# Kernel tuning notes

Hardware: AMD Instinct MI355X
Metric: run time of the kernel (lower is better)

Reference implementation:

```python
import jax, jax.numpy as jnp
import numpy as np

T = 96      # CONTEXT_SIZE
B = 32      # BATCH_SIZE
DIN = 256   # input_dim
H = 512     # hidden_dim
V = 128     # output_dim (vocab)


def setup_inputs() -> dict:
    key = jax.random.key(0)
    ks = jax.random.split(key, 16)
    s_in = 1.0 / np.sqrt(DIN)
    s_h = 1.0 / np.sqrt(H)

    def u(k, shape, s):
        return jax.random.uniform(k, shape, jnp.float32, -s, s)

    return {
        "x": jax.random.normal(ks[0], (B, T, DIN), jnp.float32),
        # input->hidden gate weights (no bias), one per timestep: [T, H, DIN]
        "Wif": u(ks[1], (T, H, DIN), s_in),
        "Wii": u(ks[2], (T, H, DIN), s_in),
        "Wic": u(ks[3], (T, H, DIN), s_in),
        "Wio": u(ks[4], (T, H, DIN), s_in),
        # hidden->hidden gate weights (+bias), one per timestep: [T, H, H], [T, H]
        "Whf_w": u(ks[5], (T, H, H), s_h), "Whf_b": u(ks[6], (T, H), s_h),
        "Whi_w": u(ks[7], (T, H, H), s_h), "Whi_b": u(ks[8], (T, H), s_h),
        "Whc_w": u(ks[9], (T, H, H), s_h), "Whc_b": u(ks[10], (T, H), s_h),
        "Who_w": u(ks[11], (T, H, H), s_h), "Who_b": u(ks[12], (T, H), s_h),
        # per-step output projections: [T, V, H], [T, V]
        "lin_w": u(ks[13], (T, V, H), s_h), "lin_b": u(ks[14], (T, V), s_h),
    }


def reference(x, Wif, Wii, Wic, Wio, Whf_w, Whf_b, Whi_w, Whi_b,
              Whc_w, Whc_b, Who_w, Who_b, lin_w, lin_b):
    sig = jax.nn.sigmoid

    # --- step 0: h_prev/c_prev are None -> hidden-path linears (and their
    # biases) are entirely absent, and c_t = i * c_bar (no forget term).
    x0 = x[:, 0]                                    # [B, DIN]
    i0 = sig(x0 @ Wii[0].T)
    cb0 = jnp.tanh(x0 @ Wic[0].T)
    o0 = sig(x0 @ Wio[0].T)
    c0 = i0 * cb0
    h0 = o0 * jnp.tanh(c0)                          # [B, H]
    logit0 = h0 @ lin_w[0].T + lin_b[0]             # [B, V]

    # --- steps 1..T-1: full gated update, distinct weights per step.
    def step(carry, ws):
        c, h = carry
        (xt, wif, whfw, whfb, wii, whiw, whib,
         wic, whcw, whcb, wio, whow, whob, lw, lb) = ws
        f = sig(xt @ wif.T + h @ whfw.T + whfb)
        i = sig(xt @ wii.T + h @ whiw.T + whib)
        cb = jnp.tanh(xt @ wic.T + h @ whcw.T + whcb)
        o = sig(xt @ wio.T + h @ whow.T + whob)
        c_t = f * c + i * cb
        h_t = o * jnp.tanh(c_t)
        return (c_t, h_t), h_t @ lw.T + lb

    xs = (jnp.swapaxes(x, 0, 1)[1:],               # [T-1, B, DIN]
          Wif[1:], Whf_w[1:], Whf_b[1:],
          Wii[1:], Whi_w[1:], Whi_b[1:],
          Wic[1:], Whc_w[1:], Whc_b[1:],
          Wio[1:], Who_w[1:], Who_b[1:],
          lin_w[1:], lin_b[1:])
    _, logits_rest = jax.lax.scan(step, (c0, h0), xs)   # [T-1, B, V]

    logits = jnp.concatenate([logit0[None], logits_rest], axis=0)  # [T, B, V]
    # original stacks [B, 1, V] per step along dim=1 -> [B, T, 1, V]
    return jnp.transpose(logits, (1, 0, 2))[:, :, None, :]
```

## Files before the change

### kernel.cpp

```cpp
#include <hip/hip_runtime.h>
#include <hip/hip_bf16.h>

#define TT 96
#define BB 32
#define DIN 256
#define HH 512
#define VV 128
#define NB 256

#define BAR() asm volatile("s_waitcnt lgkmcnt(0)\ns_barrier" ::: "memory")

__global__ __launch_bounds__(256) void phaseA_kernel(
    const float* __restrict__ x,
    const float* __restrict__ Wf, const float* __restrict__ Wi,
    const float* __restrict__ Wc, const float* __restrict__ Wo,
    float* __restrict__ Z)
{
    int bid  = blockIdx.x;
    int t    = bid >> 4;
    int tile = bid & 15;
    int g    = tile >> 2;
    int h0   = (tile & 3) * 128;
    const float* W = (g == 0) ? Wf : (g == 1) ? Wi : (g == 2) ? Wc : Wo;

    __shared__ float4 Xs4[32 * 64];
    __shared__ float4 Wc4[128 * 8];

    int tid = threadIdx.x;
    {
        int b   = tid >> 3;
        int kq8 = tid & 7;
        const float* src = x + ((size_t)b * TT + t) * DIN;
        int bx = b & 15;
        #pragma unroll
        for (int j = 0; j < 8; ++j) {
            int q = kq8 * 8 + j;
            Xs4[b * 64 + (q ^ bx)] = *reinterpret_cast<const float4*>(src + q * 4);
        }
    }

    int rg = tid >> 3;
    int bg = tid & 7;
    const float* wbase = W + ((size_t)t * HH + h0) * DIN;

    int srow[4], sgq[4];
    #pragma unroll
    for (int j = 0; j < 4; ++j) {
        int s = j * 256 + tid;
        srow[j] = s >> 3;
        sgq[j]  = (s & 7) ^ ((srow[j] >> 2) & 7);
    }

    float4 stg[4];
    #pragma unroll
    for (int j = 0; j < 4; ++j)
        stg[j] = *reinterpret_cast<const float4*>(wbase + (size_t)srow[j] * DIN + sgq[j] * 4);

    float acc[4][4];
    #pragma unroll
    for (int r = 0; r < 4; ++r)
        #pragma unroll
        for (int c = 0; c < 4; ++c) acc[r][c] = 0.f;

    for (int kc = 0; kc < 8; ++kc) {
        __syncthreads();
        #pragma unroll
        for (int j = 0; j < 4; ++j) Wc4[j * 256 + tid] = stg[j];
        __syncthreads();
        if (kc < 7) {
            #pragma unroll
            for (int j = 0; j < 4; ++j)
                stg[j] = *reinterpret_cast<const float4*>(
                    wbase + (size_t)srow[j] * DIN + (kc + 1) * 32 + sgq[j] * 4);
        }
        #pragma unroll
        for (int q = 0; q < 8; ++q) {
            float4 xv[4], wv[4];
            #pragma unroll
            for (int c = 0; c < 4; ++c) {
                int b = c * 8 + bg;
                xv[c] = Xs4[b * 64 + ((kc * 8 + q) ^ (b & 15))];
            }
            #pragma unroll
            for (int r = 0; r < 4; ++r)
                wv[r] = Wc4[(rg * 4 + r) * 8 + (q ^ (rg & 7))];
            #pragma unroll
            for (int r = 0; r < 4; ++r)
                #pragma unroll
                for (int c = 0; c < 4; ++c) {
                    acc[r][c] = fmaf(wv[r].x, xv[c].x, acc[r][c]);
                    acc[r][c] = fmaf(wv[r].y, xv[c].y, acc[r][c]);
                    acc[r][c] = fmaf(wv[r].z, xv[c].z, acc[r][c]);
                    acc[r][c] = fmaf(wv[r].w, xv[c].w, acc[r][c]);
                }
        }
    }

    size_t zbase = ((size_t)(t * 4 + g) * HH + h0 + rg * 4) * BB;
    #pragma unroll
    for (int r = 0; r < 4; ++r)
        #pragma unroll
        for (int c = 0; c < 4; ++c)
            Z[zbase + (size_t)r * BB + c * 8 + bg] = acc[r][c];
}

__global__ __launch_bounds__(512, 2) void lstm_persistent(
    const float* __restrict__ Whf, const float* __restrict__ Whi,
    const float* __restrict__ Whc, const float* __restrict__ Who,
    const float* __restrict__ bf,  const float* __restrict__ bi,
    const float* __restrict__ bc,  const float* __restrict__ bo,
    const float* __restrict__ Z,   float* __restrict__ Hall,
    unsigned* __restrict__ flags)
{
    int blk  = blockIdx.x;
    int r0   = blk * 2;
    int tid  = threadIdx.x;
    int ks   = tid >> 4;
    int bg   = tid & 15;
    int wid  = tid >> 6;
    int lane = tid & 63;

    __shared__ float pre[2][32][8][32];

    float creg = 0.f;

    for (int t = 0; t < TT; ++t) {
        int p = t & 1;

        float4 pfw[4];
        float4 pfz;
        bool pf_on = (t + 1 < TT) && (wid >= 4);
        int  idx   = tid - 256;
        if (pf_on) {
            #pragma unroll
            for (int j = 0; j < 4; ++j) {
                int f    = j * 256 + idx;
                int gate = f >> 8;
                int rl   = (f >> 7) & 1;
                int q    = f & 127;
                const float* wsrc = ((gate == 0) ? Whf : (gate == 1) ? Whi :
                                     (gate == 2) ? Whc : Who)
                                    + ((size_t)(t + 1) * HH + r0 + rl) * HH + q * 4;
                pfw[j] = *reinterpret_cast<const float4*>(wsrc);
            }
            if (idx < 64) {
                int g2 = idx >> 4, rl = (idx >> 3) & 1, qq = idx & 7;
                pfz = *reinterpret_cast<const float4*>(
                    Z + ((size_t)((t + 1) * 4 + g2) * HH + r0 + rl) * BB + qq * 4);
            }
        }

        if (t > 0) {
            {
                const unsigned* myf = flags + wid * 32 + (lane & 31);
                for (;;) {
                    unsigned v = __hip_atomic_load(myf, __ATOMIC_RELAXED,
                                                   __HIP_MEMORY_SCOPE_AGENT);
                    if (__all((int)(v >= (unsigned)t))) break;
                    __builtin_amdgcn_s_sleep(1);
                }
            }

            float a[8][2];
            #pragma unroll
            for (int rg = 0; rg < 8; ++rg) { a[rg][0] = 0.f; a[rg][1] = 0.f; }

            int k0 = ks * 16;
            const float* hbase = Hall + (size_t)(t - 1) * HH * BB + (size_t)k0 * BB + 2 * bg;
            const float* wp[8];
            #pragma unroll
            for (int rl = 0; rl < 2; ++rl) {
                size_t wo = ((size_t)t * HH + r0 + rl) * HH + k0;
                wp[rl * 4 + 0] = Whf + wo;
                wp[rl * 4 + 1] = Whi + wo;
                wp[rl * 4 + 2] = Whc + wo;
                wp[rl * 4 + 3] = Who + wo;
            }
            #pragma unroll
            for (int q = 0; q < 4; ++q) {
                float2 hv[4];
                #pragma unroll
                for (int j = 0; j < 4; ++j)
                    hv[j] = *reinterpret_cast<const float2*>(hbase + (size_t)(q * 4 + j) * BB);
                #pragma unroll
                for (int rg = 0; rg < 8; ++rg) {
                    float4 w = *reinterpret_cast<const float4*>(wp[rg] + q * 4);
                    a[rg][0] = fmaf(w.x, hv[0].x, a[rg][0]); a[rg][1] = fmaf(w.x, hv[0].y, a[rg][1]);
                    a[rg][0] = fmaf(w.y, hv[1].x, a[rg][0]); a[rg][1] = fmaf(w.y, hv[1].y, a[rg][1]);
                    a[rg][0] = fmaf(w.z, hv[2].x, a[rg][0]); a[rg][1] = fmaf(w.z, hv[2].y, a[rg][1]);
                    a[rg][0] = fmaf(w.w, hv[3].x, a[rg][0]); a[rg][1] = fmaf(w.w, hv[3].y, a[rg][1]);
                }
            }
            #pragma unroll
            for (int rg = 0; rg < 8; ++rg) {
                pre[p][ks][rg][2 * bg]     = a[rg][0];
                pre[p][ks][rg][2 * bg + 1] = a[rg][1];
            }
        }

        if (pf_on) {
            float s = pfw[0].x + pfw[0].y + pfw[0].z + pfw[0].w
                    + pfw[1].x + pfw[1].y + pfw[1].z + pfw[1].w
                    + pfw[2].x + pfw[2].y + pfw[2].z + pfw[2].w
                    + pfw[3].x + pfw[3].y + pfw[3].z + pfw[3].w;
            if (idx < 64) s += pfz.x + pfz.y + pfz.z + pfz.w;
            asm volatile("" :: "v"(s));
        }

        BAR();

        if (wid == 0) {
            int rl  = lane >> 5;
            int b   = lane & 31;
            int row = r0 + rl;
            float s0 = 0.f, s1 = 0.f, s2 = 0.f, s3 = 0.f;
            if (t > 0) {
                #pragma unroll
                for (int k2 = 0; k2 < 32; ++k2) {
                    s0 += pre[p][k2][rl * 4 + 0][b];
                    s1 += pre[p][k2][rl * 4 + 1][b];
                    s2 += pre[p][k2][rl * 4 + 2][b];
                    s3 += pre[p][k2][rl * 4 + 3][b];
                }
                s0 += bf[t * HH + row];
                s1 += bi[t * HH + row];
                s2 += bc[t * HH + row];
                s3 += bo[t * HH + row];
            }
            s0 += Z[((size_t)(t * 4 + 0) * HH + row) * BB + b];
            s1 += Z[((size_t)(t * 4 + 1) * HH + row) * BB + b];
            s2 += Z[((size_t)(t * 4 + 2) * HH + row) * BB + b];
            s3 += Z[((size_t)(t * 4 + 3) * HH + row) * BB + b];

            float f  = 1.f / (1.f + __expf(-s0));
            float i  = 1.f / (1.f + __expf(-s1));
            float cb = tanhf(s2);
            float o  = 1.f / (1.f + __expf(-s3));
            float cn = f * creg + i * cb;
            creg = cn;
            float hn = o * tanhf(cn);

            __hip_atomic_store(Hall + ((size_t)t * HH + row) * BB + b, hn,
                               __ATOMIC_RELAXED, __HIP_MEMORY_SCOPE_AGENT);
            asm volatile("s_waitcnt vmcnt(0)" ::: "memory");
            if (lane == 0)
                __hip_atomic_store(&flags[blk], (unsigned)(t + 1),
                                   __ATOMIC_RELAXED, __HIP_MEMORY_SCOPE_AGENT);
        }
    }
}

__global__ __launch_bounds__(256) void phaseC_kernel(
    const float* __restrict__ lw, const float* __restrict__ lb,
    const float* __restrict__ Hall, float* __restrict__ out)
{
    int t  = blockIdx.x >> 2;
    int v0 = (blockIdx.x & 3) << 5;
    int tid = threadIdx.x;
    int v  = v0 + (tid >> 3);
    int bg = tid & 7;
    const float* w  = lw + ((size_t)t * VV + v) * HH;
    const float* hp = Hall + (size_t)t * HH * BB;
    float acc0 = 0.f, acc1 = 0.f, acc2 = 0.f, acc3 = 0.f;
    #pragma unroll 4
    for (int k = 0; k < HH; ++k) {
        float wv = w[k];
        float4 hv = *reinterpret_cast<const float4*>(hp + (size_t)k * BB + bg * 4);
        acc0 = fmaf(wv, hv.x, acc0);
        acc1 = fmaf(wv, hv.y, acc1);
        acc2 = fmaf(wv, hv.z, acc2);
        acc3 = fmaf(wv, hv.w, acc3);
    }
    float bias = lb[t * VV + v];
    float r[4] = {acc0 + bias, acc1 + bias, acc2 + bias, acc3 + bias};
    #pragma unroll
    for (int j = 0; j < 4; ++j) {
        int b = bg * 4 + j;
        out[((size_t)b * TT + t) * VV + v] = r[j];
    }
}

extern "C" void kernel_launch(void* const* d_in, const int* in_sizes, int n_in,
                              void* d_out, int out_size, void* d_ws, size_t ws_size,
                              hipStream_t stream)
{
    const float* x     = (const float*)d_in[0];
    const float* Wif   = (const float*)d_in[1];
    const float* Wii   = (const float*)d_in[2];
    const float* Wic   = (const float*)d_in[3];
    const float* Wio   = (const float*)d_in[4];
    const float* Whf_w = (const float*)d_in[5];
    const float* Whf_b = (const float*)d_in[6];
    const float* Whi_w = (const float*)d_in[7];
    const float* Whi_b = (const float*)d_in[8];
    const float* Whc_w = (const float*)d_in[9];
    const float* Whc_b = (const float*)d_in[10];
    const float* Who_w = (const float*)d_in[11];
    const float* Who_b = (const float*)d_in[12];
    const float* lin_w = (const float*)d_in[13];
    const float* lin_b = (const float*)d_in[14];
    float* out = (float*)d_out;

    float*    Z     = (float*)d_ws;
    float*    Hall  = Z + (size_t)TT * 4 * HH * BB;
    unsigned* flags = (unsigned*)(Hall + (size_t)TT * HH * BB);

    hipMemsetAsync(flags, 0, NB * sizeof(unsigned), stream);

    phaseA_kernel<<<dim3(TT * 16), dim3(256), 0, stream>>>(x, Wif, Wii, Wic, Wio, Z);

    lstm_persistent<<<dim3(NB), dim3(512), 0, stream>>>(
        Whf_w, Whi_w, Whc_w, Who_w, Whf_b, Whi_b, Whc_b, Who_b, Z, Hall, flags);

    phaseC_kernel<<<dim3(TT * 4), dim3(256), 0, stream>>>(lin_w, lin_b, Hall, out);
}
```

Measured before the change: 974.2 us.

## Replace per-block flag handshake with tagged 64-bit hidden-state words

Each hidden value is stored together with its timestep tag in one 64-bit atomic word, so consumers spin by reading the data itself and checking the tags instead of polling separate flags. This removes the store-then-wait-then-flag sequence and one polling round trip per step on the recurrent critical path. In exchange the hidden-state buffer doubles in size, must be zeroed by a large memset each launch, and the output projection reads twice the bytes. A retry repeats the whole partial dot product.

```diff
diff --git a/kernel.cpp b/kernel.cpp
--- a/kernel.cpp
+++ b/kernel.cpp
@@ -109,8 +109,7 @@
     const float* __restrict__ Whc, const float* __restrict__ Who,
     const float* __restrict__ bf,  const float* __restrict__ bi,
     const float* __restrict__ bc,  const float* __restrict__ bo,
-    const float* __restrict__ Z,   float* __restrict__ Hall,
-    unsigned* __restrict__ flags)
+    const float* __restrict__ Z,   unsigned long long* __restrict__ Hall2)
 {
     int blk  = blockIdx.x;
     int r0   = blk * 2;
@@ -151,22 +150,9 @@
         }
 
         if (t > 0) {
-            {
-                const unsigned* myf = flags + wid * 32 + (lane & 31);
-                for (;;) {
-                    unsigned v = __hip_atomic_load(myf, __ATOMIC_RELAXED,
-                                                   __HIP_MEMORY_SCOPE_AGENT);
-                    if (__all((int)(v >= (unsigned)t))) break;
-                    __builtin_amdgcn_s_sleep(1);
-                }
-            }
-
-            float a[8][2];
-            #pragma unroll
-            for (int rg = 0; rg < 8; ++rg) { a[rg][0] = 0.f; a[rg][1] = 0.f; }
-
             int k0 = ks * 16;
-            const float* hbase = Hall + (size_t)(t - 1) * HH * BB + (size_t)k0 * BB + 2 * bg;
+            const unsigned long long* hp =
+                Hall2 + (size_t)(t - 1) * HH * BB + (size_t)k0 * BB + 2 * bg;
             const float* wp[8];
             #pragma unroll
             for (int rl = 0; rl < 2; ++rl) {
@@ -176,20 +162,42 @@
                 wp[rl * 4 + 2] = Whc + wo;
                 wp[rl * 4 + 3] = Who + wo;
             }
-            #pragma unroll
-            for (int q = 0; q < 4; ++q) {
-                float2 hv[4];
+            unsigned tagexp = (unsigned)t;
+            float a[8][2];
+            for (;;) {
+                bool ok = true;
                 #pragma unroll
-                for (int j = 0; j < 4; ++j)
-                    hv[j] = *reinterpret_cast<const float2*>(hbase + (size_t)(q * 4 + j) * BB);
+                for (int rg = 0; rg < 8; ++rg) { a[rg][0] = 0.f; a[rg][1] = 0.f; }
                 #pragma unroll
-                for (int rg = 0; rg < 8; ++rg) {
-                    float4 w = *reinterpret_cast<const float4*>(wp[rg] + q * 4);
-                    a[rg][0] = fmaf(w.x, hv[0].x, a[rg][0]); a[rg][1] = fmaf(w.x, hv[0].y, a[rg][1]);
-                    a[rg][0] = fmaf(w.y, hv[1].x, a[rg][0]); a[rg][1] = fmaf(w.y, hv[1].y, a[rg][1]);
-                    a[rg][0] = fmaf(w.z, hv[2].x, a[rg][0]); a[rg][1] = fmaf(w.z, hv[2].y, a[rg][1]);
-                    a[rg][0] = fmaf(w.w, hv[3].x, a[rg][0]); a[rg][1] = fmaf(w.w, hv[3].y, a[rg][1]);
+                for (int q = 0; q < 4; ++q) {
+                    unsigned long long u0[4], u1[4];
+                    #pragma unroll
+                    for (int j = 0; j < 4; ++j) {
+                        const unsigned long long* rowp = hp + (size_t)(q * 4 + j) * BB;
+                        u0[j] = __hip_atomic_load(rowp,     __ATOMIC_RELAXED,
+                                                  __HIP_MEMORY_SCOPE_AGENT);
+                        u1[j] = __hip_atomic_load(rowp + 1, __ATOMIC_RELAXED,
+                                                  __HIP_MEMORY_SCOPE_AGENT);
+                    }
+                    float2 hv[4];
+                    #pragma unroll
+                    for (int j = 0; j < 4; ++j) {
+                        ok = ok && ((unsigned)(u0[j] >> 32) == tagexp)
+                                && ((unsigned)(u1[j] >> 32) == tagexp);
+                        hv[j].x = __uint_as_float((unsigned)u0[j]);
+                        hv[j].y = __uint_as_float((unsigned)u1[j]);
+                    }
+                    #pragma unroll
+                    for (int rg = 0; rg < 8; ++rg) {
+                        float4 w = *reinterpret_cast<const float4*>(wp[rg] + q * 4);
+                        a[rg][0] = fmaf(w.x, hv[0].x, a[rg][0]); a[rg][1] = fmaf(w.x, hv[0].y, a[rg][1]);
+                        a[rg][0] = fmaf(w.y, hv[1].x, a[rg][0]); a[rg][1] = fmaf(w.y, hv[1].y, a[rg][1]);
+                        a[rg][0] = fmaf(w.z, hv[2].x, a[rg][0]); a[rg][1] = fmaf(w.z, hv[2].y, a[rg][1]);
+                        a[rg][0] = fmaf(w.w, hv[3].x, a[rg][0]); a[rg][1] = fmaf(w.w, hv[3].y, a[rg][1]);
+                    }
                 }
+                if (__all(ok)) break;
+                __builtin_amdgcn_s_sleep(1);
             }
             #pragma unroll
             for (int rg = 0; rg < 8; ++rg) {
@@ -240,36 +248,36 @@
             creg = cn;
             float hn = o * tanhf(cn);
 
-            __hip_atomic_store(Hall + ((size_t)t * HH + row) * BB + b, hn,
+            unsigned long long pair =
+                ((unsigned long long)(unsigned)(t + 1) << 32) | __float_as_uint(hn);
+            __hip_atomic_store(Hall2 + ((size_t)t * HH + row) * BB + b, pair,
                                __ATOMIC_RELAXED, __HIP_MEMORY_SCOPE_AGENT);
-            asm volatile("s_waitcnt vmcnt(0)" ::: "memory");
-            if (lane == 0)
-                __hip_atomic_store(&flags[blk], (unsigned)(t + 1),
-                                   __ATOMIC_RELAXED, __HIP_MEMORY_SCOPE_AGENT);
         }
     }
 }
 
 __global__ __launch_bounds__(256) void phaseC_kernel(
     const float* __restrict__ lw, const float* __restrict__ lb,
-    const float* __restrict__ Hall, float* __restrict__ out)
+    const unsigned long long* __restrict__ Hall2, float* __restrict__ out)
 {
     int t  = blockIdx.x >> 2;
     int v0 = (blockIdx.x & 3) << 5;
     int tid = threadIdx.x;
     int v  = v0 + (tid >> 3);
     int bg = tid & 7;
-    const float* w  = lw + ((size_t)t * VV + v) * HH;
-    const float* hp = Hall + (size_t)t * HH * BB;
+    const float* w = lw + ((size_t)t * VV + v) * HH;
+    const unsigned long long* hp = Hall2 + (size_t)t * HH * BB;
     float acc0 = 0.f, acc1 = 0.f, acc2 = 0.f, acc3 = 0.f;
     #pragma unroll 4
     for (int k = 0; k < HH; ++k) {
         float wv = w[k];
-        float4 hv = *reinterpret_cast<const float4*>(hp + (size_t)k * BB + bg * 4);
-        acc0 = fmaf(wv, hv.x, acc0);
-        acc1 = fmaf(wv, hv.y, acc1);
-        acc2 = fmaf(wv, hv.z, acc2);
-        acc3 = fmaf(wv, hv.w, acc3);
+        const float4* pp = reinterpret_cast<const float4*>(hp + (size_t)k * BB + bg * 4);
+        float4 a0 = pp[0];
+        float4 a1 = pp[1];
+        acc0 = fmaf(wv, a0.x, acc0);
+        acc1 = fmaf(wv, a0.z, acc1);
+        acc2 = fmaf(wv, a1.x, acc2);
+        acc3 = fmaf(wv, a1.z, acc3);
     }
     float bias = lb[t * VV + v];
     float r[4] = {acc0 + bias, acc1 + bias, acc2 + bias, acc3 + bias};
@@ -301,16 +309,16 @@
     const float* lin_b = (const float*)d_in[14];
     float* out = (float*)d_out;
 
-    float*    Z     = (float*)d_ws;
-    float*    Hall  = Z + (size_t)TT * 4 * HH * BB;
-    unsigned* flags = (unsigned*)(Hall + (size_t)TT * HH * BB);
-
-    hipMemsetAsync(flags, 0, NB * sizeof(unsigned), stream);
+    float* Z = (float*)d_ws;
+    unsigned long long* Hall2 =
+        (unsigned long long*)(Z + (size_t)TT * 4 * HH * BB);
+
+    hipMemsetAsync(Hall2, 0, (size_t)TT * HH * BB * sizeof(unsigned long long), stream);
 
     phaseA_kernel<<<dim3(TT * 16), dim3(256), 0, stream>>>(x, Wif, Wii, Wic, Wio, Z);
 
     lstm_persistent<<<dim3(NB), dim3(512), 0, stream>>>(
-        Whf_w, Whi_w, Whc_w, Who_w, Whf_b, Whi_b, Whc_b, Who_b, Z, Hall, flags);
-
-    phaseC_kernel<<<dim3(TT * 4), dim3(256), 0, stream>>>(lin_w, lin_b, Hall, out);
+        Whf_w, Whi_w, Whc_w, Who_w, Whf_b, Whi_b, Whc_b, Who_b, Z, Hall2);
+
+    phaseC_kernel<<<dim3(TT * 4), dim3(256), 0, stream>>>(lin_w, lin_b, Hall2, out);
 }
```

Result: slower. 1.296 ms (+33.0%).
